# Kernel optimization log

Hardware: AMD Instinct MI355X
Metric: run time of the kernel (lower is better)

## Reference

```python
import jax, jax.numpy as jnp
import numpy as np

B, S, HID = 2, 2048, 3584
H, KV, D = 16, 8, 256
RQ, RK, RV = 6, 2, 2
GRP = H // KV
EPS = 1e-6
SOFTCAP = 50.0
SCALE = 256.0 ** -0.5  # query_pre_attn_scalar ** -0.5
NEG = -2.3819763e38


def _rmsnorm(x, w):
    # Gemma RMSNorm: fp32 normalize, scale by (1 + weight)
    xf = x.astype(jnp.float32)
    n = xf * jax.lax.rsqrt(jnp.mean(xf * xf, axis=-1, keepdims=True) + EPS)
    return (n * (1.0 + w)).astype(x.dtype)


def _rope_factor(x, freqs_cis):
    # x: [B,S,R,D]; freqs_cis: [S, D/2, 2] = (cos, sin)
    h = D // 2
    cos = freqs_cis[None, :, None, :, 0]  # [1,S,1,D/2]
    sin = freqs_cis[None, :, None, :, 1]
    x1, x2 = x[..., :h], x[..., h:]
    return jnp.concatenate([x1 * cos - x2 * sin, x2 * cos + x1 * sin], axis=-1)


def setup_inputs() -> dict:
    key = jax.random.key(0)
    ks = jax.random.split(key, 10)
    hidden_states = jax.random.normal(ks[0], (B, S, HID), dtype=jnp.float32)
    # rotary tables
    pos = jnp.arange(S, dtype=jnp.float32)
    inv = 1.0 / (10000.0 ** (jnp.arange(0, D, 2, dtype=jnp.float32) / D))
    ang = pos[:, None] * inv[None, :]                     # [S, D/2]
    freqs_cis = jnp.stack([jnp.cos(ang), jnp.sin(ang)], axis=-1)  # [S,D/2,2]
    kv_write_indices = jnp.arange(S, dtype=jnp.int32)
    k_cache_A = jnp.zeros((B, S, KV, RK), jnp.float32)
    k_cache_B = jnp.zeros((B, S, RK, D), jnp.float32)
    v_cache_A = jnp.zeros((B, S, KV, RV), jnp.float32)
    v_cache_B = jnp.zeros((B, S, RV, D), jnp.float32)
    causal = jnp.tril(jnp.ones((S, S), bool))
    mask = jnp.where(causal, 0.0, NEG)[None, None].astype(jnp.float32)
    sd = 1.0 / np.sqrt(HID)
    W_A_q = jax.random.normal(ks[1], (HID, H * RQ), jnp.float32) * sd
    W_A_k = jax.random.normal(ks[2], (HID, KV * RK), jnp.float32) * sd
    W_A_v = jax.random.normal(ks[3], (HID, KV * RV), jnp.float32) * sd
    W_B_q = jax.random.normal(ks[4], (HID, RQ * D), jnp.float32) * sd
    W_B_k = jax.random.normal(ks[5], (HID, RK * D), jnp.float32) * sd
    W_B_v = jax.random.normal(ks[6], (HID, RV * D), jnp.float32) * sd
    o_proj_w = jax.random.normal(ks[7], (H * D, HID), jnp.float32) * (1.0 / np.sqrt(H * D))
    q_norm_w = jnp.zeros((D,), jnp.float32)
    k_norm_w = jnp.zeros((D,), jnp.float32)
    return dict(hidden_states=hidden_states, freqs_cis=freqs_cis,
                kv_write_indices=kv_write_indices,
                k_cache_A=k_cache_A, k_cache_B=k_cache_B,
                v_cache_A=v_cache_A, v_cache_B=v_cache_B, mask=mask,
                W_A_q=W_A_q, W_A_k=W_A_k, W_A_v=W_A_v,
                W_B_q=W_B_q, W_B_k=W_B_k, W_B_v=W_B_v,
                o_proj_w=o_proj_w, q_norm_w=q_norm_w, k_norm_w=k_norm_w)


def reference(hidden_states, freqs_cis, kv_write_indices,
              k_cache_A, k_cache_B, v_cache_A, v_cache_B, mask,
              W_A_q, W_A_k, W_A_v, W_B_q, W_B_k, W_B_v,
              o_proj_w, q_norm_w, k_norm_w):
    hs = hidden_states
    # rank-factor projections (many small GEMMs)
    A_q = (hs @ W_A_q).reshape(B, S, H, RQ)
    A_k = (hs @ W_A_k).reshape(B, S, KV, RK)
    A_v = (hs @ W_A_v).reshape(B, S, KV, RV)
    B_q = (hs @ W_B_q).reshape(B, S, RQ, D)
    B_k = (hs @ W_B_k).reshape(B, S, RK, D)
    B_v = (hs @ W_B_v).reshape(B, S, RV, D)
    # qk-norm on low-rank B factors
    B_q = _rmsnorm(B_q, q_norm_w)
    B_k = _rmsnorm(B_k, k_norm_w)
    # RoPE on factors
    B_q = _rope_factor(B_q, freqs_cis)
    B_k = _rope_factor(B_k, freqs_cis)
    # factored KV cache write (prefill: indices = arange(S))
    kA = k_cache_A.at[:, kv_write_indices].set(A_k)
    kB = k_cache_B.at[:, kv_write_indices].set(B_k)
    vA = v_cache_A.at[:, kv_write_indices].set(A_v)
    vB = v_cache_B.at[:, kv_write_indices].set(B_v)
    # reconstruct Q/K/V from rank-R tensor products, divided by rank
    Q = jnp.einsum('bshr,bsrd->bshd', A_q.astype(jnp.float32),
                   B_q.astype(jnp.float32)) / RQ          # [B,S,H,D]
    K = jnp.einsum('bskr,bsrd->bskd', kA, kB) / RK        # [B,S,KV,D]
    V = jnp.einsum('bskr,bsrd->bskd', vA, vB) / RV
    Q = Q.astype(hs.dtype)
    # GQA expand
    K = jnp.repeat(K, GRP, axis=2)
    V = jnp.repeat(V, GRP, axis=2)
    q = jnp.transpose(Q, (0, 2, 1, 3)) * SCALE            # [B,H,S,D]
    k = jnp.transpose(K, (0, 2, 1, 3))
    v = jnp.transpose(V, (0, 2, 1, 3))
    scores = jnp.einsum('bhqd,bhkd->bhqk', q, k).astype(jnp.float32)
    scores = SOFTCAP * jnp.tanh(scores / SOFTCAP)
    scores = scores + mask
    probs = jax.nn.softmax(scores, axis=-1).astype(q.dtype)
    out = jnp.einsum('bhqk,bhkd->bhqd', probs, v)         # [B,H,S,D]
    out = jnp.transpose(out, (0, 2, 1, 3)).reshape(B, S, H * D)
    return out @ o_proj_w
```

## Files before the change

### kernel.cpp

```cpp
#include <hip/hip_runtime.h>

#define B_    2
#define S_    2048
#define HID_  3584
#define H_    16
#define KV_   8
#define D_    256
#define RQ_   6
#define NPROJ 2688
#define HD_   4096
#define MTOK  4096
#define EPS_  1e-6f
#define NEG_  -2.3819763e38f
#define SCALE_ 0.0625f

typedef unsigned short u16;
typedef __attribute__((ext_vector_type(8))) short short8;
typedef __attribute__((ext_vector_type(4))) float f32x4;

__device__ __forceinline__ u16 f2bf(float f) {
  unsigned u = __float_as_uint(f);
  u += 0x7fffu + ((u >> 16) & 1u);
  return (u16)(u >> 16);
}

__device__ __forceinline__ void gl_lds16(const void* g, void* l) {
  __builtin_amdgcn_global_load_lds((__attribute__((address_space(1))) void*)g,
                                   (__attribute__((address_space(3))) void*)l, 16, 0, 0);
}

__global__ __launch_bounds__(256) void cvt_f32_bf16(const float* __restrict__ src,
                                                    u16* __restrict__ dst, int n) {
  int i = blockIdx.x * 256 + threadIdx.x;
  const int stride = gridDim.x * 256;
  const int n4 = n >> 2;
  for (; i < n4; i += stride) {
    float4 v = ((const float4*)src)[i];
    ushort4 o;
    o.x = f2bf(v.x); o.y = f2bf(v.y); o.z = f2bf(v.z); o.w = f2bf(v.w);
    ((ushort4*)dst)[i] = o;
  }
}

__global__ __launch_bounds__(256) void transpose_f32_bf16(const float* __restrict__ src,
                                                          u16* __restrict__ dst, int R, int C) {
  __shared__ float tile[32][33];
  const int tx = threadIdx.x & 31, ty = threadIdx.x >> 5;
  const int r0 = blockIdx.x << 5, c0 = blockIdx.y << 5;
#pragma unroll
  for (int j = 0; j < 4; ++j) {
    int r = r0 + ty + j * 8, c = c0 + tx;
    tile[ty + j * 8][tx] = (r < R && c < C) ? src[(size_t)r * C + c] : 0.f;
  }
  __syncthreads();
#pragma unroll
  for (int j = 0; j < 4; ++j) {
    int cc = c0 + ty + j * 8, rr = r0 + tx;
    if (cc < C && rr < R) dst[(size_t)cc * R + rr] = f2bf(tile[tx][ty + j * 8]);
  }
}

__global__ __launch_bounds__(256) void transpose_bf16_b(const u16* __restrict__ src,
                                                        u16* __restrict__ dst, int R, int C) {
  __shared__ u16 tile[32][34];
  const size_t plane = (size_t)R * C;
  const u16* s = src + (size_t)blockIdx.z * plane;
  u16* d = dst + (size_t)blockIdx.z * plane;
  const int tx = threadIdx.x & 31, ty = threadIdx.x >> 5;
  const int r0 = blockIdx.x << 5, c0 = blockIdx.y << 5;
#pragma unroll
  for (int j = 0; j < 4; ++j) {
    int r = r0 + ty + j * 8, c = c0 + tx;
    tile[ty + j * 8][tx] = (r < R && c < C) ? s[(size_t)r * C + c] : (u16)0;
  }
  __syncthreads();
#pragma unroll
  for (int j = 0; j < 4; ++j) {
    int cc = c0 + ty + j * 8, rr = r0 + tx;
    if (cc < C && rr < R) d[(size_t)cc * R + rr] = tile[tx][ty + j * 8];
  }
}

__global__ __launch_bounds__(512, 2)
void gemm256(const u16* __restrict__ A, const u16* __restrict__ Bm, float* __restrict__ C,
             int N, int lda, int ldb, int ldc, int NT) {
  __shared__ __align__(16) u16 lds[2][2][2][8192];
  const int t = threadIdx.x;
  const int lane = t & 63;
  const int lq = lane & 15, lg = lane >> 4;
  const int w = t >> 6;
  const int wm = w >> 2, wn = w & 3;
  const int bm0 = blockIdx.x * 256, bn0 = blockIdx.y * 256;

  const int rsub = lane >> 2;
  const int ksub = (((lane & 3) ^ ((lane >> 3) & 3)) << 3);
  const u16* pa0 = A + (size_t)(bm0 + w * 16 + rsub) * lda + ksub;
  const u16* pa1 = pa0 + (size_t)128 * lda;
  const u16* pb0 = Bm + (size_t)(bn0 + w * 16 + rsub) * ldb + ksub;
  const u16* pb1 = pb0 + (size_t)128 * ldb;

  const int rdo = lq * 32 + ((lg ^ ((lq >> 1) & 3)) << 3);
  const int bsub = (wn & 1) << 3;

  f32x4 zero = {0.f, 0.f, 0.f, 0.f};
  f32x4 acc[8][4];
#pragma unroll
  for (int m = 0; m < 8; ++m)
#pragma unroll
    for (int n = 0; n < 4; ++n) acc[m][n] = zero;

  gl_lds16(pa0,      &lds[0][0][0][(w * 2 + 0) * 512]);
  gl_lds16(pa1,      &lds[0][0][1][(w * 2 + 0) * 512]);
  gl_lds16(pb0,      &lds[0][1][0][(w * 2 + 0) * 512]);
  gl_lds16(pb1,      &lds[0][1][1][(w * 2 + 0) * 512]);
  gl_lds16(pa0 + 32, &lds[0][0][0][(w * 2 + 1) * 512]);
  gl_lds16(pa1 + 32, &lds[0][0][1][(w * 2 + 1) * 512]);
  gl_lds16(pb0 + 32, &lds[0][1][0][(w * 2 + 1) * 512]);
  gl_lds16(pb1 + 32, &lds[0][1][1][(w * 2 + 1) * 512]);

  int cur = 0;
  for (int T = 0; T < NT; ++T) {
    const bool pre = (T + 1) < NT;
    const size_t ko = (size_t)(T + 1) * 64;
    const u16* ab = &lds[cur][0][wm][0];
    const u16* bb = &lds[cur][1][wn >> 1][0];
    const int nb = cur ^ 1;

    asm volatile("s_waitcnt vmcnt(4)" ::: "memory");
    __builtin_amdgcn_s_barrier();
    __builtin_amdgcn_sched_barrier(0);
    short8 af[4], bf[4];
#pragma unroll
    for (int m = 0; m < 4; ++m) af[m] = *(const short8*)(ab + (m * 2 + 0) * 512 + rdo);
#pragma unroll
    for (int n = 0; n < 4; ++n) bf[n] = *(const short8*)(bb + (bsub + n * 2 + 0) * 512 + rdo);
    if (pre) {
      gl_lds16(pa0 + ko, &lds[nb][0][0][(w * 2 + 0) * 512]);
      gl_lds16(pa1 + ko, &lds[nb][0][1][(w * 2 + 0) * 512]);
    }
    __builtin_amdgcn_s_setprio(1);
#pragma unroll
    for (int m = 0; m < 4; ++m)
#pragma unroll
      for (int n = 0; n < 4; ++n)
        acc[m][n] = __builtin_amdgcn_mfma_f32_16x16x32_bf16(af[m], bf[n], acc[m][n], 0, 0, 0);
    __builtin_amdgcn_s_setprio(0);

    short8 ag[4];
#pragma unroll
    for (int m = 0; m < 4; ++m) ag[m] = *(const short8*)(ab + ((m + 4) * 2 + 0) * 512 + rdo);
    if (pre) {
      gl_lds16(pb0 + ko, &lds[nb][1][0][(w * 2 + 0) * 512]);
      gl_lds16(pb1 + ko, &lds[nb][1][1][(w * 2 + 0) * 512]);
    }
    __builtin_amdgcn_s_setprio(1);
#pragma unroll
    for (int m = 0; m < 4; ++m)
#pragma unroll
      for (int n = 0; n < 4; ++n)
        acc[m + 4][n] = __builtin_amdgcn_mfma_f32_16x16x32_bf16(ag[m], bf[n], acc[m + 4][n], 0, 0, 0);
    __builtin_amdgcn_s_setprio(0);

    if (pre) { asm volatile("s_waitcnt vmcnt(4)" ::: "memory"); }
    else     { asm volatile("s_waitcnt vmcnt(0)" ::: "memory"); }
    __builtin_amdgcn_s_barrier();
    __builtin_amdgcn_sched_barrier(0);
    short8 af2[4], bf2[4];
#pragma unroll
    for (int m = 0; m < 4; ++m) af2[m] = *(const short8*)(ab + (m * 2 + 1) * 512 + rdo);
#pragma unroll
    for (int n = 0; n < 4; ++n) bf2[n] = *(const short8*)(bb + (bsub + n * 2 + 1) * 512 + rdo);
    if (pre) {
      gl_lds16(pa0 + ko + 32, &lds[nb][0][0][(w * 2 + 1) * 512]);
      gl_lds16(pa1 + ko + 32, &lds[nb][0][1][(w * 2 + 1) * 512]);
    }
    __builtin_amdgcn_s_setprio(1);
#pragma unroll
    for (int m = 0; m < 4; ++m)
#pragma unroll
      for (int n = 0; n < 4; ++n)
        acc[m][n] = __builtin_amdgcn_mfma_f32_16x16x32_bf16(af2[m], bf2[n], acc[m][n], 0, 0, 0);
    __builtin_amdgcn_s_setprio(0);

    short8 ag2[4];
#pragma unroll
    for (int m = 0; m < 4; ++m) ag2[m] = *(const short8*)(ab + ((m + 4) * 2 + 1) * 512 + rdo);
    if (pre) {
      gl_lds16(pb0 + ko + 32, &lds[nb][1][0][(w * 2 + 1) * 512]);
      gl_lds16(pb1 + ko + 32, &lds[nb][1][1][(w * 2 + 1) * 512]);
    }
    __builtin_amdgcn_s_setprio(1);
#pragma unroll
    for (int m = 0; m < 4; ++m)
#pragma unroll
      for (int n = 0; n < 4; ++n)
        acc[m + 4][n] = __builtin_amdgcn_mfma_f32_16x16x32_bf16(ag2[m], bf2[n], acc[m + 4][n], 0, 0, 0);
    __builtin_amdgcn_s_setprio(0);

    cur ^= 1;
  }

#pragma unroll
  for (int m = 0; m < 8; ++m) {
    const int row = bm0 + wm * 128 + m * 16 + lg * 4;
#pragma unroll
    for (int n = 0; n < 4; ++n) {
      const int col = bn0 + wn * 64 + n * 16 + lq;
      if (col < N) {
        float* cp = C + (size_t)row * ldc + col;
        cp[0] = acc[m][n][0];
        cp[(size_t)ldc] = acc[m][n][1];
        cp[(size_t)2 * ldc] = acc[m][n][2];
        cp[(size_t)3 * ldc] = acc[m][n][3];
      }
    }
  }
}

__global__ __launch_bounds__(256)
void build_qkv(const float* __restrict__ P, const float* __restrict__ freqs,
               const float* __restrict__ qw, const float* __restrict__ kw,
               u16* __restrict__ Qg, u16* __restrict__ Kg, u16* __restrict__ Vg) {
  const int token = blockIdx.x;
  const int b = token >> 11, s = token & 2047;
  const int d = threadIdx.x;
  const float* row = P + (size_t)token * NPROJ;
  __shared__ float aL[128];
  __shared__ float rQ[6][256];
  __shared__ float rK[2][256];
  __shared__ float red[4][8];

  if (d < 128) aL[d] = row[d];
  float bq[6], bk[2], bv[2];
#pragma unroll
  for (int r = 0; r < 6; ++r) bq[r] = row[128 + r * 256 + d];
#pragma unroll
  for (int r = 0; r < 2; ++r) bk[r] = row[1664 + r * 256 + d];
#pragma unroll
  for (int r = 0; r < 2; ++r) bv[r] = row[2176 + r * 256 + d];

  float sq[8];
#pragma unroll
  for (int r = 0; r < 6; ++r) sq[r] = bq[r] * bq[r];
  sq[6] = bk[0] * bk[0];
  sq[7] = bk[1] * bk[1];
#pragma unroll
  for (int j = 0; j < 8; ++j) {
    sq[j] += __shfl_xor(sq[j], 32, 64);
    sq[j] += __shfl_xor(sq[j], 16, 64);
    sq[j] += __shfl_xor(sq[j], 8, 64);
    sq[j] += __shfl_xor(sq[j], 4, 64);
    sq[j] += __shfl_xor(sq[j], 2, 64);
    sq[j] += __shfl_xor(sq[j], 1, 64);
  }
  const int lane = d & 63, wv = d >> 6;
  if (lane == 0) {
#pragma unroll
    for (int j = 0; j < 8; ++j) red[wv][j] = sq[j];
  }
  __syncthreads();
  float inv[8];
#pragma unroll
  for (int j = 0; j < 8; ++j) {
    float ss = red[0][j] + red[1][j] + red[2][j] + red[3][j];
    inv[j] = rsqrtf(ss * (1.0f / 256.0f) + EPS_);
  }
  const float gq = 1.f + qw[d], gk = 1.f + kw[d];
#pragma unroll
  for (int r = 0; r < 6; ++r) rQ[r][d] = bq[r] * inv[r] * gq;
#pragma unroll
  for (int r = 0; r < 2; ++r) rK[r][d] = bk[r] * inv[6 + r] * gk;
  __syncthreads();

  const int dh = d & 127;
  const float co = freqs[(s * 128 + dh) * 2 + 0];
  const float sn = freqs[(s * 128 + dh) * 2 + 1];
  float q_ro[6], k_ro[2];
  if (d < 128) {
#pragma unroll
    for (int r = 0; r < 6; ++r) q_ro[r] = rQ[r][d] * co - rQ[r][d + 128] * sn;
#pragma unroll
    for (int r = 0; r < 2; ++r) k_ro[r] = rK[r][d] * co - rK[r][d + 128] * sn;
  } else {
#pragma unroll
    for (int r = 0; r < 6; ++r) q_ro[r] = rQ[r][d] * co + rQ[r][d - 128] * sn;
#pragma unroll
    for (int r = 0; r < 2; ++r) k_ro[r] = rK[r][d] * co + rK[r][d - 128] * sn;
  }
  const float qs = SCALE_ * (1.0f / 6.0f);
#pragma unroll
  for (int h = 0; h < 16; ++h) {
    float a = 0.f;
#pragma unroll
    for (int r = 0; r < 6; ++r) a += aL[h * 6 + r] * q_ro[r];
    Qg[((size_t)(b * H_ + h) * S_ + s) * D_ + d] = f2bf(a * qs);
  }
#pragma unroll
  for (int kv = 0; kv < 8; ++kv) {
    float ak = aL[96 + kv * 2] * k_ro[0] + aL[96 + kv * 2 + 1] * k_ro[1];
    Kg[((size_t)(b * KV_ + kv) * S_ + s) * D_ + d] = f2bf(ak * 0.5f);
    float av = aL[112 + kv * 2] * bv[0] + aL[112 + kv * 2 + 1] * bv[1];
    Vg[((size_t)(b * KV_ + kv) * S_ + s) * D_ + d] = f2bf(av * 0.5f);
  }
}

__global__ __launch_bounds__(256, 2)
void attn_kernel(const u16* __restrict__ Qg, const u16* __restrict__ Kg,
                 const u16* __restrict__ VTg, u16* __restrict__ Og) {
  __shared__ __align__(16) u16 Kbuf[2][8192];
  __shared__ __align__(16) u16 Vbuf[2][8192];
  __shared__ __align__(16) u16 Pbuf[4][512];

  const int t = threadIdx.x;
  const int lane = t & 63;
  const int lq = lane & 15, lg = lane >> 4;
  const int qw = t >> 6;
  const int h = blockIdx.x, b = blockIdx.y;
  const int qt = 31 - blockIdx.z;
  const int q0 = qt * 64;
  const int kvh = h >> 1;

  const u16* Kplane = Kg + (size_t)(b * KV_ + kvh) * S_ * D_;
  const u16* VTplane = VTg + (size_t)(b * KV_ + kvh) * D_ * S_;

  const int qg = q0 + qw * 16 + lq;
  const u16* Qrow = Qg + ((size_t)(b * H_ + h) * S_ + qg) * D_;
  short8 qf[8];
#pragma unroll
  for (int ks = 0; ks < 8; ++ks) qf[ks] = *(const short8*)(Qrow + ks * 32 + lg * 8);

  int ksrc[4], vsrc[4];
#pragma unroll
  for (int i = 0; i < 4; ++i) {
    const int kr = i * 8 + (t >> 5);
    ksrc[i] = kr * D_ + (((t & 31) ^ (kr & 7)) << 3);
    const int vr = i * 64 + (t >> 2);
    vsrc[i] = vr * S_ + (((t & 3) ^ ((vr >> 1) & 3)) << 3);
  }

  f32x4 zero = {0.f, 0.f, 0.f, 0.f};
  f32x4 oacc[16];
#pragma unroll
  for (int db = 0; db < 16; ++db) oacc[db] = zero;
  float m_s = NEG_, l_s = 0.f;

  const int qro = q0 + qw * 16 + lg * 4;
  const int nt = 2 * (qt + 1);

#pragma unroll
  for (int i = 0; i < 4; ++i) {
    gl_lds16(Kplane + ksrc[i], &Kbuf[0][0] + (i * 256 + t) * 8);
    gl_lds16(VTplane + vsrc[i], &Vbuf[0][0] + (i * 256 + t) * 8);
  }
  __syncthreads();
  int cur = 0;
  for (int it = 0; it < nt; ++it) {
    const int kv0 = it * 32;
    if (it + 1 < nt) {
      const u16* kp = Kplane + (size_t)(it + 1) * 32 * D_;
      const u16* vp = VTplane + (it + 1) * 32;
      u16* kd = &Kbuf[cur ^ 1][0];
      u16* vd = &Vbuf[cur ^ 1][0];
#pragma unroll
      for (int i = 0; i < 4; ++i) {
        gl_lds16(kp + ksrc[i], kd + (i * 256 + t) * 8);
        gl_lds16(vp + vsrc[i], vd + (i * 256 + t) * 8);
      }
    }
    const u16* Kb = &Kbuf[cur][0];
    f32x4 sacc[2];
    sacc[0] = zero; sacc[1] = zero;
    __builtin_amdgcn_s_setprio(1);
#pragma unroll
    for (int kb = 0; kb < 2; ++kb) {
      const int rbase = (kb * 16 + lq) * 256;
      const int sw = lq & 7;
#pragma unroll
      for (int ks = 0; ks < 8; ++ks) {
        short8 kf = *(const short8*)(Kb + rbase + (((ks * 4 + lg) ^ sw) << 3));
        sacc[kb] = __builtin_amdgcn_mfma_f32_16x16x32_bf16(kf, qf[ks], sacc[kb], 0, 0, 0);
      }
    }
    __builtin_amdgcn_s_setprio(0);
    const bool tail = (it >= 2 * qt);
#pragma unroll
    for (int kb = 0; kb < 2; ++kb)
#pragma unroll
      for (int r = 0; r < 4; ++r) {
        float x = sacc[kb][r];
        const float e = __expf(-fabsf(x) * 0.04f);
        const float th = (1.f - e) * __builtin_amdgcn_rcpf(1.f + e);
        x = copysignf(50.0f * th, x);
        if (tail && (kv0 + kb * 16 + lg * 4 + r > qg)) x = NEG_;
        sacc[kb][r] = x;
      }
    float vmax = fmaxf(fmaxf(fmaxf(sacc[0][0], sacc[0][1]), fmaxf(sacc[0][2], sacc[0][3])),
                       fmaxf(fmaxf(sacc[1][0], sacc[1][1]), fmaxf(sacc[1][2], sacc[1][3])));
    vmax = fmaxf(vmax, __shfl_xor(vmax, 16, 64));
    vmax = fmaxf(vmax, __shfl_xor(vmax, 32, 64));
    if (__any(vmax > m_s + 8.f)) {
      const float mn = fmaxf(m_s, vmax);
      const float c = __expf(m_s - mn);
      m_s = mn;
      l_s *= c;
      float c4[4];
#pragma unroll
      for (int r = 0; r < 4; ++r) c4[r] = __shfl(c, lg * 4 + r, 16);
#pragma unroll
      for (int db = 0; db < 16; ++db) {
        oacc[db][0] *= c4[0]; oacc[db][1] *= c4[1];
        oacc[db][2] *= c4[2]; oacc[db][3] *= c4[3];
      }
    }
    float ps = 0.f;
#pragma unroll
    for (int kb = 0; kb < 2; ++kb)
#pragma unroll
      for (int r = 0; r < 4; ++r) {
        const float p = __expf(sacc[kb][r] - m_s);
        sacc[kb][r] = p;
        ps += p;
      }
    ps += __shfl_xor(ps, 16, 64);
    ps += __shfl_xor(ps, 32, 64);
    l_s += ps;
    u16* Pw = &Pbuf[qw][0];
#pragma unroll
    for (int kb = 0; kb < 2; ++kb) {
      ushort4 pk;
      pk.x = f2bf(sacc[kb][0]); pk.y = f2bf(sacc[kb][1]);
      pk.z = f2bf(sacc[kb][2]); pk.w = f2bf(sacc[kb][3]);
      *(ushort4*)(Pw + 8 * lq + 128 * (2 * kb + (lg >> 1)) + 4 * (lg & 1)) = pk;
    }
    short8 pf = *(const short8*)(Pw + lane * 8);
    const u16* Vb = &Vbuf[cur][0];
    __builtin_amdgcn_s_setprio(1);
#pragma unroll
    for (int db = 0; db < 16; ++db) {
      const int d = db * 16 + lq;
      short8 vf = *(const short8*)(Vb + d * 32 + ((lg ^ ((lq >> 1) & 3)) << 3));
      oacc[db] = __builtin_amdgcn_mfma_f32_16x16x32_bf16(pf, vf, oacc[db], 0, 0, 0);
    }
    __builtin_amdgcn_s_setprio(0);
    __syncthreads();
    cur ^= 1;
  }
  const float invl = __builtin_amdgcn_rcpf(l_s);
  float inv4[4];
#pragma unroll
  for (int r = 0; r < 4; ++r) inv4[r] = __shfl(invl, lg * 4 + r, 16);
#pragma unroll
  for (int r = 0; r < 4; ++r) {
    u16* orow = Og + (size_t)(b * S_ + qro + r) * HD_ + h * D_;
#pragma unroll
    for (int db = 0; db < 16; ++db) orow[db * 16 + lq] = f2bf(oacc[db][r] * inv4[r]);
  }
}

extern "C" void kernel_launch(void* const* d_in, const int* in_sizes, int n_in,
                              void* d_out, int out_size, void* d_ws, size_t ws_size,
                              hipStream_t stream) {
  const float* hs    = (const float*)d_in[0];
  const float* freqs = (const float*)d_in[1];
  const float* W_A_q = (const float*)d_in[8];
  const float* W_A_k = (const float*)d_in[9];
  const float* W_A_v = (const float*)d_in[10];
  const float* W_B_q = (const float*)d_in[11];
  const float* W_B_k = (const float*)d_in[12];
  const float* W_B_v = (const float*)d_in[13];
  const float* Wo    = (const float*)d_in[14];
  const float* qw    = (const float*)d_in[15];
  const float* kw    = (const float*)d_in[16];
  float* out = (float*)d_out;

  char* ws = (char*)d_ws;
  u16* hsb = (u16*)(ws);
  u16* WT  = (u16*)(ws + 29360128);
  u16* WoT = (u16*)(ws + 48627712);
  u16* Qg  = (u16*)(ws + 77987840);
  u16* Kg  = (u16*)(ws + 111542272);
  u16* Vg  = (u16*)(ws + 128319488);
  u16* VTg = (u16*)(ws + 145096704);
  u16* AOg = (u16*)(ws + 161873920);
  float* Pout = (float*)d_out;

  cvt_f32_bf16<<<1024, 256, 0, stream>>>(hs, hsb, MTOK * HID_);
  transpose_f32_bf16<<<dim3(112, 3),   256, 0, stream>>>(W_A_q, WT + (size_t)0 * HID_,    HID_, 96);
  transpose_f32_bf16<<<dim3(112, 1),   256, 0, stream>>>(W_A_k, WT + (size_t)96 * HID_,   HID_, 16);
  transpose_f32_bf16<<<dim3(112, 1),   256, 0, stream>>>(W_A_v, WT + (size_t)112 * HID_,  HID_, 16);
  transpose_f32_bf16<<<dim3(112, 48),  256, 0, stream>>>(W_B_q, WT + (size_t)128 * HID_,  HID_, 1536);
  transpose_f32_bf16<<<dim3(112, 16),  256, 0, stream>>>(W_B_k, WT + (size_t)1664 * HID_, HID_, 512);
  transpose_f32_bf16<<<dim3(112, 16),  256, 0, stream>>>(W_B_v, WT + (size_t)2176 * HID_, HID_, 512);
  transpose_f32_bf16<<<dim3(128, 112), 256, 0, stream>>>(Wo, WoT, HD_, HID_);

  gemm256<<<dim3(16, 11), 512, 0, stream>>>(hsb, WT, Pout, NPROJ, HID_, HID_, NPROJ, 56);
  build_qkv<<<4096, 256, 0, stream>>>(Pout, freqs, qw, kw, Qg, Kg, Vg);
  transpose_bf16_b<<<dim3(64, 8, 16), 256, 0, stream>>>(Vg, VTg, S_, D_);
  attn_kernel<<<dim3(16, 2, 32), 256, 0, stream>>>(Qg, Kg, VTg, AOg);
  gemm256<<<dim3(16, 14), 512, 0, stream>>>(AOg, WoT, out, HID_, HD_, HD_, HID_, 64);
}
```

Measured before the change: 431.9 us.

## Double attention query tile per block to reuse K/V tiles across two row groups

```diff
diff --git a/kernel.cpp b/kernel.cpp
--- a/kernel.cpp
+++ b/kernel.cpp
@@ -309,25 +309,28 @@
                  const u16* __restrict__ VTg, u16* __restrict__ Og) {
   __shared__ __align__(16) u16 Kbuf[2][8192];
   __shared__ __align__(16) u16 Vbuf[2][8192];
-  __shared__ __align__(16) u16 Pbuf[4][512];
+  __shared__ __align__(16) u16 Pbuf[4][1024];
 
   const int t = threadIdx.x;
   const int lane = t & 63;
   const int lq = lane & 15, lg = lane >> 4;
   const int qw = t >> 6;
   const int h = blockIdx.x, b = blockIdx.y;
-  const int qt = 31 - blockIdx.z;
-  const int q0 = qt * 64;
+  const int qt = 15 - blockIdx.z;
+  const int q0 = qt * 128;
   const int kvh = h >> 1;
+  const int qbase = q0 + qw * 32;
 
   const u16* Kplane = Kg + (size_t)(b * KV_ + kvh) * S_ * D_;
   const u16* VTplane = VTg + (size_t)(b * KV_ + kvh) * D_ * S_;
 
-  const int qg = q0 + qw * 16 + lq;
-  const u16* Qrow = Qg + ((size_t)(b * H_ + h) * S_ + qg) * D_;
-  short8 qf[8];
-#pragma unroll
-  for (int ks = 0; ks < 8; ++ks) qf[ks] = *(const short8*)(Qrow + ks * 32 + lg * 8);
+  short8 qf[2][8];
+#pragma unroll
+  for (int qh = 0; qh < 2; ++qh) {
+    const u16* Qrow = Qg + ((size_t)(b * H_ + h) * S_ + qbase + qh * 16 + lq) * D_;
+#pragma unroll
+    for (int ks = 0; ks < 8; ++ks) qf[qh][ks] = *(const short8*)(Qrow + ks * 32 + lg * 8);
+  }
 
   int ksrc[4], vsrc[4];
 #pragma unroll
@@ -339,13 +342,14 @@
   }
 
   f32x4 zero = {0.f, 0.f, 0.f, 0.f};
-  f32x4 oacc[16];
-#pragma unroll
-  for (int db = 0; db < 16; ++db) oacc[db] = zero;
-  float m_s = NEG_, l_s = 0.f;
-
-  const int qro = q0 + qw * 16 + lg * 4;
-  const int nt = 2 * (qt + 1);
+  f32x4 oacc[2][16];
+#pragma unroll
+  for (int qh = 0; qh < 2; ++qh)
+#pragma unroll
+    for (int db = 0; db < 16; ++db) oacc[qh][db] = zero;
+  float m_s[2] = {NEG_, NEG_}, l_s[2] = {0.f, 0.f};
+
+  const int nt = 4 * qt + 4;
 
 #pragma unroll
   for (int i = 0; i < 4; ++i) {
@@ -367,93 +371,118 @@
         gl_lds16(vp + vsrc[i], vd + (i * 256 + t) * 8);
       }
     }
-    const u16* Kb = &Kbuf[cur][0];
-    f32x4 sacc[2];
-    sacc[0] = zero; sacc[1] = zero;
-    __builtin_amdgcn_s_setprio(1);
-#pragma unroll
-    for (int kb = 0; kb < 2; ++kb) {
-      const int rbase = (kb * 16 + lq) * 256;
-      const int sw = lq & 7;
-#pragma unroll
-      for (int ks = 0; ks < 8; ++ks) {
-        short8 kf = *(const short8*)(Kb + rbase + (((ks * 4 + lg) ^ sw) << 3));
-        sacc[kb] = __builtin_amdgcn_mfma_f32_16x16x32_bf16(kf, qf[ks], sacc[kb], 0, 0, 0);
-      }
-    }
-    __builtin_amdgcn_s_setprio(0);
-    const bool tail = (it >= 2 * qt);
-#pragma unroll
-    for (int kb = 0; kb < 2; ++kb)
-#pragma unroll
-      for (int r = 0; r < 4; ++r) {
-        float x = sacc[kb][r];
-        const float e = __expf(-fabsf(x) * 0.04f);
-        const float th = (1.f - e) * __builtin_amdgcn_rcpf(1.f + e);
-        x = copysignf(50.0f * th, x);
-        if (tail && (kv0 + kb * 16 + lg * 4 + r > qg)) x = NEG_;
-        sacc[kb][r] = x;
-      }
-    float vmax = fmaxf(fmaxf(fmaxf(sacc[0][0], sacc[0][1]), fmaxf(sacc[0][2], sacc[0][3])),
-                       fmaxf(fmaxf(sacc[1][0], sacc[1][1]), fmaxf(sacc[1][2], sacc[1][3])));
-    vmax = fmaxf(vmax, __shfl_xor(vmax, 16, 64));
-    vmax = fmaxf(vmax, __shfl_xor(vmax, 32, 64));
-    if (__any(vmax > m_s + 8.f)) {
-      const float mn = fmaxf(m_s, vmax);
-      const float c = __expf(m_s - mn);
-      m_s = mn;
-      l_s *= c;
-      float c4[4];
-#pragma unroll
-      for (int r = 0; r < 4; ++r) c4[r] = __shfl(c, lg * 4 + r, 16);
+    if (kv0 <= qbase + 31) {
+      const u16* Kb = &Kbuf[cur][0];
+      f32x4 sacc[2][2];
+      sacc[0][0] = zero; sacc[0][1] = zero; sacc[1][0] = zero; sacc[1][1] = zero;
+      __builtin_amdgcn_s_setprio(1);
+#pragma unroll
+      for (int kb = 0; kb < 2; ++kb) {
+        const int rbase = (kb * 16 + lq) * 256;
+        const int sw = lq & 7;
+#pragma unroll
+        for (int ks = 0; ks < 8; ++ks) {
+          short8 kf = *(const short8*)(Kb + rbase + (((ks * 4 + lg) ^ sw) << 3));
+          sacc[0][kb] = __builtin_amdgcn_mfma_f32_16x16x32_bf16(kf, qf[0][ks], sacc[0][kb], 0, 0, 0);
+          sacc[1][kb] = __builtin_amdgcn_mfma_f32_16x16x32_bf16(kf, qf[1][ks], sacc[1][kb], 0, 0, 0);
+        }
+      }
+      __builtin_amdgcn_s_setprio(0);
+      float vmax[2];
+#pragma unroll
+      for (int qh = 0; qh < 2; ++qh) {
+        const int qg = qbase + qh * 16 + lq;
+        const bool tail = (kv0 + 31 > qbase + qh * 16);
+        float vm = NEG_;
+#pragma unroll
+        for (int kb = 0; kb < 2; ++kb)
+#pragma unroll
+          for (int r = 0; r < 4; ++r) {
+            float x = sacc[qh][kb][r];
+            const float e = __expf(-fabsf(x) * 0.04f);
+            const float th = (1.f - e) * __builtin_amdgcn_rcpf(1.f + e);
+            x = copysignf(50.0f * th, x);
+            if (tail && (kv0 + kb * 16 + lg * 4 + r > qg)) x = NEG_;
+            sacc[qh][kb][r] = x;
+            vm = fmaxf(vm, x);
+          }
+        vm = fmaxf(vm, __shfl_xor(vm, 16, 64));
+        vm = fmaxf(vm, __shfl_xor(vm, 32, 64));
+        vmax[qh] = vm;
+      }
+      const bool grow = (vmax[0] > m_s[0] + 8.f) | (vmax[1] > m_s[1] + 8.f);
+      if (__any(grow)) {
+        float c4[2][4];
+#pragma unroll
+        for (int qh = 0; qh < 2; ++qh) {
+          const float mn = fmaxf(m_s[qh], vmax[qh]);
+          const float c = __expf(m_s[qh] - mn);
+          m_s[qh] = mn;
+          l_s[qh] *= c;
+#pragma unroll
+          for (int r = 0; r < 4; ++r) c4[qh][r] = __shfl(c, lg * 4 + r, 16);
+        }
+#pragma unroll
+        for (int qh = 0; qh < 2; ++qh)
+#pragma unroll
+          for (int db = 0; db < 16; ++db) {
+            oacc[qh][db][0] *= c4[qh][0]; oacc[qh][db][1] *= c4[qh][1];
+            oacc[qh][db][2] *= c4[qh][2]; oacc[qh][db][3] *= c4[qh][3];
+          }
+      }
+#pragma unroll
+      for (int qh = 0; qh < 2; ++qh) {
+        float ps = 0.f;
+#pragma unroll
+        for (int kb = 0; kb < 2; ++kb)
+#pragma unroll
+          for (int r = 0; r < 4; ++r) {
+            const float p = __expf(sacc[qh][kb][r] - m_s[qh]);
+            sacc[qh][kb][r] = p;
+            ps += p;
+          }
+        ps += __shfl_xor(ps, 16, 64);
+        ps += __shfl_xor(ps, 32, 64);
+        l_s[qh] += ps;
+      }
+      u16* Pw = &Pbuf[qw][0];
+#pragma unroll
+      for (int qh = 0; qh < 2; ++qh)
+#pragma unroll
+        for (int kb = 0; kb < 2; ++kb) {
+          ushort4 pk;
+          pk.x = f2bf(sacc[qh][kb][0]); pk.y = f2bf(sacc[qh][kb][1]);
+          pk.z = f2bf(sacc[qh][kb][2]); pk.w = f2bf(sacc[qh][kb][3]);
+          *(ushort4*)(Pw + qh * 512 + 8 * lq + 128 * (2 * kb + (lg >> 1)) + 4 * (lg & 1)) = pk;
+        }
+      short8 pf0 = *(const short8*)(Pw + lane * 8);
+      short8 pf1 = *(const short8*)(Pw + 512 + lane * 8);
+      const u16* Vb = &Vbuf[cur][0];
+      __builtin_amdgcn_s_setprio(1);
 #pragma unroll
       for (int db = 0; db < 16; ++db) {
-        oacc[db][0] *= c4[0]; oacc[db][1] *= c4[1];
-        oacc[db][2] *= c4[2]; oacc[db][3] *= c4[3];
-      }
-    }
-    float ps = 0.f;
-#pragma unroll
-    for (int kb = 0; kb < 2; ++kb)
-#pragma unroll
-      for (int r = 0; r < 4; ++r) {
-        const float p = __expf(sacc[kb][r] - m_s);
-        sacc[kb][r] = p;
-        ps += p;
-      }
-    ps += __shfl_xor(ps, 16, 64);
-    ps += __shfl_xor(ps, 32, 64);
-    l_s += ps;
-    u16* Pw = &Pbuf[qw][0];
-#pragma unroll
-    for (int kb = 0; kb < 2; ++kb) {
-      ushort4 pk;
-      pk.x = f2bf(sacc[kb][0]); pk.y = f2bf(sacc[kb][1]);
-      pk.z = f2bf(sacc[kb][2]); pk.w = f2bf(sacc[kb][3]);
-      *(ushort4*)(Pw + 8 * lq + 128 * (2 * kb + (lg >> 1)) + 4 * (lg & 1)) = pk;
-    }
-    short8 pf = *(const short8*)(Pw + lane * 8);
-    const u16* Vb = &Vbuf[cur][0];
-    __builtin_amdgcn_s_setprio(1);
-#pragma unroll
-    for (int db = 0; db < 16; ++db) {
-      const int d = db * 16 + lq;
-      short8 vf = *(const short8*)(Vb + d * 32 + ((lg ^ ((lq >> 1) & 3)) << 3));
-      oacc[db] = __builtin_amdgcn_mfma_f32_16x16x32_bf16(pf, vf, oacc[db], 0, 0, 0);
-    }
-    __builtin_amdgcn_s_setprio(0);
+        const int d = db * 16 + lq;
+        short8 vf = *(const short8*)(Vb + d * 32 + ((lg ^ ((lq >> 1) & 3)) << 3));
+        oacc[0][db] = __builtin_amdgcn_mfma_f32_16x16x32_bf16(pf0, vf, oacc[0][db], 0, 0, 0);
+        oacc[1][db] = __builtin_amdgcn_mfma_f32_16x16x32_bf16(pf1, vf, oacc[1][db], 0, 0, 0);
+      }
+      __builtin_amdgcn_s_setprio(0);
+    }
     __syncthreads();
     cur ^= 1;
   }
-  const float invl = __builtin_amdgcn_rcpf(l_s);
-  float inv4[4];
-#pragma unroll
-  for (int r = 0; r < 4; ++r) inv4[r] = __shfl(invl, lg * 4 + r, 16);
-#pragma unroll
-  for (int r = 0; r < 4; ++r) {
-    u16* orow = Og + (size_t)(b * S_ + qro + r) * HD_ + h * D_;
-#pragma unroll
-    for (int db = 0; db < 16; ++db) orow[db * 16 + lq] = f2bf(oacc[db][r] * inv4[r]);
+#pragma unroll
+  for (int qh = 0; qh < 2; ++qh) {
+    const float invl = __builtin_amdgcn_rcpf(l_s[qh]);
+    float inv4[4];
+#pragma unroll
+    for (int r = 0; r < 4; ++r) inv4[r] = __shfl(invl, lg * 4 + r, 16);
+#pragma unroll
+    for (int r = 0; r < 4; ++r) {
+      u16* orow = Og + (size_t)(b * S_ + qbase + qh * 16 + lg * 4 + r) * HD_ + h * D_;
+#pragma unroll
+      for (int db = 0; db < 16; ++db) orow[db * 16 + lq] = f2bf(oacc[qh][db][r] * inv4[r]);
+    }
   }
 }
 
@@ -496,6 +525,6 @@
   gemm256<<<dim3(16, 11), 512, 0, stream>>>(hsb, WT, Pout, NPROJ, HID_, HID_, NPROJ, 56);
   build_qkv<<<4096, 256, 0, stream>>>(Pout, freqs, qw, kw, Qg, Kg, Vg);
   transpose_bf16_b<<<dim3(64, 8, 16), 256, 0, stream>>>(Vg, VTg, S_, D_);
-  attn_kernel<<<dim3(16, 2, 32), 256, 0, stream>>>(Qg, Kg, VTg, AOg);
+  attn_kernel<<<dim3(16, 2, 16), 256, 0, stream>>>(Qg, Kg, VTg, AOg);
   gemm256<<<dim3(16, 14), 512, 0, stream>>>(AOg, WoT, out, HID_, HD_, HD_, HID_, 64);
 }
```

New measurement: 477.3 us. +10.5%, slower.

## Use four-stage K ring with one barrier per step and XCD-aware tile remap

Applied to the files above, without the earlier changes.

```diff
diff --git a/kernel.cpp b/kernel.cpp
--- a/kernel.cpp
+++ b/kernel.cpp
@@ -81,26 +81,27 @@
   }
 }
 
-__global__ __launch_bounds__(512, 2)
+__global__ __launch_bounds__(512, 1)
 void gemm256(const u16* __restrict__ A, const u16* __restrict__ Bm, float* __restrict__ C,
-             int N, int lda, int ldb, int ldc, int NT) {
-  __shared__ __align__(16) u16 lds[2][2][2][8192];
+             int N, int lda, int ldb, int ldc, int NT, int GY) {
+  __shared__ __align__(16) u16 ring[4][2][8192];
   const int t = threadIdx.x;
   const int lane = t & 63;
   const int lq = lane & 15, lg = lane >> 4;
   const int w = t >> 6;
   const int wm = w >> 2, wn = w & 3;
-  const int bm0 = blockIdx.x * 256, bn0 = blockIdx.y * 256;
+
+  const int wg = blockIdx.x;
+  const int chunk = gridDim.x >> 3;
+  const int gid = (wg & 7) * chunk + (wg >> 3);
+  const int bm0 = (gid / GY) * 256, bn0 = (gid % GY) * 256;
 
   const int rsub = lane >> 2;
   const int ksub = (((lane & 3) ^ ((lane >> 3) & 3)) << 3);
-  const u16* pa0 = A + (size_t)(bm0 + w * 16 + rsub) * lda + ksub;
-  const u16* pa1 = pa0 + (size_t)128 * lda;
-  const u16* pb0 = Bm + (size_t)(bn0 + w * 16 + rsub) * ldb + ksub;
-  const u16* pb1 = pb0 + (size_t)128 * ldb;
+  const u16* paw = A + (size_t)(bm0 + w * 32 + rsub) * lda + ksub;
+  const u16* pbw = Bm + (size_t)(bn0 + w * 32 + rsub) * ldb + ksub;
 
   const int rdo = lq * 32 + ((lg ^ ((lq >> 1) & 3)) << 3);
-  const int bsub = (wn & 1) << 3;
 
   f32x4 zero = {0.f, 0.f, 0.f, 0.f};
   f32x4 acc[8][4];
@@ -109,96 +110,47 @@
 #pragma unroll
     for (int n = 0; n < 4; ++n) acc[m][n] = zero;
 
-  gl_lds16(pa0,      &lds[0][0][0][(w * 2 + 0) * 512]);
-  gl_lds16(pa1,      &lds[0][0][1][(w * 2 + 0) * 512]);
-  gl_lds16(pb0,      &lds[0][1][0][(w * 2 + 0) * 512]);
-  gl_lds16(pb1,      &lds[0][1][1][(w * 2 + 0) * 512]);
-  gl_lds16(pa0 + 32, &lds[0][0][0][(w * 2 + 1) * 512]);
-  gl_lds16(pa1 + 32, &lds[0][0][1][(w * 2 + 1) * 512]);
-  gl_lds16(pb0 + 32, &lds[0][1][0][(w * 2 + 1) * 512]);
-  gl_lds16(pb1 + 32, &lds[0][1][1][(w * 2 + 1) * 512]);
-
-  int cur = 0;
+#define STAGE_(T)                                                              \
+  {                                                                            \
+    const int slot_ = (T) & 3;                                                 \
+    const size_t ko_ = (size_t)(T) * 32;                                       \
+    gl_lds16(paw + ko_,            &ring[slot_][0][(2 * w + 0) * 512]);        \
+    gl_lds16(paw + 16 * lda + ko_, &ring[slot_][0][(2 * w + 1) * 512]);        \
+    gl_lds16(pbw + ko_,            &ring[slot_][1][(2 * w + 0) * 512]);        \
+    gl_lds16(pbw + 16 * ldb + ko_, &ring[slot_][1][(2 * w + 1) * 512]);        \
+  }
+
+  STAGE_(0);
+  STAGE_(1);
+  STAGE_(2);
+  asm volatile("s_waitcnt vmcnt(8)" ::: "memory");
+  __builtin_amdgcn_s_barrier();
+
   for (int T = 0; T < NT; ++T) {
-    const bool pre = (T + 1) < NT;
-    const size_t ko = (size_t)(T + 1) * 64;
-    const u16* ab = &lds[cur][0][wm][0];
-    const u16* bb = &lds[cur][1][wn >> 1][0];
-    const int nb = cur ^ 1;
-
-    asm volatile("s_waitcnt vmcnt(4)" ::: "memory");
-    __builtin_amdgcn_s_barrier();
     __builtin_amdgcn_sched_barrier(0);
-    short8 af[4], bf[4];
-#pragma unroll
-    for (int m = 0; m < 4; ++m) af[m] = *(const short8*)(ab + (m * 2 + 0) * 512 + rdo);
-#pragma unroll
-    for (int n = 0; n < 4; ++n) bf[n] = *(const short8*)(bb + (bsub + n * 2 + 0) * 512 + rdo);
-    if (pre) {
-      gl_lds16(pa0 + ko, &lds[nb][0][0][(w * 2 + 0) * 512]);
-      gl_lds16(pa1 + ko, &lds[nb][0][1][(w * 2 + 0) * 512]);
-    }
+    const int s = T & 3;
+    const u16* as = &ring[s][0][wm * 4096];
+    const u16* bs = &ring[s][1][wn * 2048];
+    short8 af[8], bf[4];
+#pragma unroll
+    for (int m = 0; m < 8; ++m) af[m] = *(const short8*)(as + m * 512 + rdo);
+#pragma unroll
+    for (int n = 0; n < 4; ++n) bf[n] = *(const short8*)(bs + n * 512 + rdo);
+    if (T + 3 < NT) STAGE_(T + 3);
     __builtin_amdgcn_s_setprio(1);
 #pragma unroll
-    for (int m = 0; m < 4; ++m)
+    for (int m = 0; m < 8; ++m)
 #pragma unroll
       for (int n = 0; n < 4; ++n)
         acc[m][n] = __builtin_amdgcn_mfma_f32_16x16x32_bf16(af[m], bf[n], acc[m][n], 0, 0, 0);
     __builtin_amdgcn_s_setprio(0);
-
-    short8 ag[4];
-#pragma unroll
-    for (int m = 0; m < 4; ++m) ag[m] = *(const short8*)(ab + ((m + 4) * 2 + 0) * 512 + rdo);
-    if (pre) {
-      gl_lds16(pb0 + ko, &lds[nb][1][0][(w * 2 + 0) * 512]);
-      gl_lds16(pb1 + ko, &lds[nb][1][1][(w * 2 + 0) * 512]);
-    }
-    __builtin_amdgcn_s_setprio(1);
-#pragma unroll
-    for (int m = 0; m < 4; ++m)
-#pragma unroll
-      for (int n = 0; n < 4; ++n)
-        acc[m + 4][n] = __builtin_amdgcn_mfma_f32_16x16x32_bf16(ag[m], bf[n], acc[m + 4][n], 0, 0, 0);
-    __builtin_amdgcn_s_setprio(0);
-
-    if (pre) { asm volatile("s_waitcnt vmcnt(4)" ::: "memory"); }
-    else     { asm volatile("s_waitcnt vmcnt(0)" ::: "memory"); }
+    if (T + 3 < NT)      { asm volatile("s_waitcnt vmcnt(8) lgkmcnt(0)" ::: "memory"); }
+    else if (T + 2 < NT) { asm volatile("s_waitcnt vmcnt(4) lgkmcnt(0)" ::: "memory"); }
+    else if (T + 1 < NT) { asm volatile("s_waitcnt vmcnt(0) lgkmcnt(0)" ::: "memory"); }
+    else                 { asm volatile("s_waitcnt lgkmcnt(0)" ::: "memory"); }
     __builtin_amdgcn_s_barrier();
-    __builtin_amdgcn_sched_barrier(0);
-    short8 af2[4], bf2[4];
-#pragma unroll
-    for (int m = 0; m < 4; ++m) af2[m] = *(const short8*)(ab + (m * 2 + 1) * 512 + rdo);
-#pragma unroll
-    for (int n = 0; n < 4; ++n) bf2[n] = *(const short8*)(bb + (bsub + n * 2 + 1) * 512 + rdo);
-    if (pre) {
-      gl_lds16(pa0 + ko + 32, &lds[nb][0][0][(w * 2 + 1) * 512]);
-      gl_lds16(pa1 + ko + 32, &lds[nb][0][1][(w * 2 + 1) * 512]);
-    }
-    __builtin_amdgcn_s_setprio(1);
-#pragma unroll
-    for (int m = 0; m < 4; ++m)
-#pragma unroll
-      for (int n = 0; n < 4; ++n)
-        acc[m][n] = __builtin_amdgcn_mfma_f32_16x16x32_bf16(af2[m], bf2[n], acc[m][n], 0, 0, 0);
-    __builtin_amdgcn_s_setprio(0);
-
-    short8 ag2[4];
-#pragma unroll
-    for (int m = 0; m < 4; ++m) ag2[m] = *(const short8*)(ab + ((m + 4) * 2 + 1) * 512 + rdo);
-    if (pre) {
-      gl_lds16(pb0 + ko + 32, &lds[nb][1][0][(w * 2 + 1) * 512]);
-      gl_lds16(pb1 + ko + 32, &lds[nb][1][1][(w * 2 + 1) * 512]);
-    }
-    __builtin_amdgcn_s_setprio(1);
-#pragma unroll
-    for (int m = 0; m < 4; ++m)
-#pragma unroll
-      for (int n = 0; n < 4; ++n)
-        acc[m + 4][n] = __builtin_amdgcn_mfma_f32_16x16x32_bf16(ag2[m], bf2[n], acc[m + 4][n], 0, 0, 0);
-    __builtin_amdgcn_s_setprio(0);
-
-    cur ^= 1;
-  }
+  }
+#undef STAGE_
 
 #pragma unroll
   for (int m = 0; m < 8; ++m) {
@@ -493,9 +445,9 @@
   transpose_f32_bf16<<<dim3(112, 16),  256, 0, stream>>>(W_B_v, WT + (size_t)2176 * HID_, HID_, 512);
   transpose_f32_bf16<<<dim3(128, 112), 256, 0, stream>>>(Wo, WoT, HD_, HID_);
 
-  gemm256<<<dim3(16, 11), 512, 0, stream>>>(hsb, WT, Pout, NPROJ, HID_, HID_, NPROJ, 56);
+  gemm256<<<176, 512, 0, stream>>>(hsb, WT, Pout, NPROJ, HID_, HID_, NPROJ, 112, 11);
   build_qkv<<<4096, 256, 0, stream>>>(Pout, freqs, qw, kw, Qg, Kg, Vg);
   transpose_bf16_b<<<dim3(64, 8, 16), 256, 0, stream>>>(Vg, VTg, S_, D_);
   attn_kernel<<<dim3(16, 2, 32), 256, 0, stream>>>(Qg, Kg, VTg, AOg);
-  gemm256<<<dim3(16, 14), 512, 0, stream>>>(AOg, WoT, out, HID_, HD_, HD_, HID_, 64);
-}
+  gemm256<<<224, 512, 0, stream>>>(AOg, WoT, out, HID_, HD_, HD_, HID_, 128, 14);
+}
```

New measurement: 440.1 us. No clear change (+1.9%).
